# Optimization experiments

Measured on AMD Instinct MI355X. Metric: run time of the kernel, lower is better.

Reference implementation:

```python
import jax, jax.numpy as jnp
import numpy as np

B, T, D = 64, 512, 1024
VOCAB = 50257


def setup_inputs() -> dict:
    key = jax.random.key(0)
    k1, k2, k3, k4 = jax.random.split(key, 4)
    vector_sequence = jax.random.normal(k1, (B, T, D), dtype=jnp.float32)
    # lengths in [1, T] to avoid degenerate all-zero rows (divide-by-zero, as in torch)
    sentence_length = jax.random.randint(k2, (B,), 1, T + 1, dtype=jnp.int32)
    word_sequence = jax.random.randint(k3, (B, T), 0, VOCAB, dtype=jnp.int32)
    # original init: 0.1 - 0.2*U[0,1) -> uniform in (-0.1, 0.1]
    weights = 0.1 - 0.2 * jax.random.uniform(k4, (VOCAB,), dtype=jnp.float32)
    return {
        "vector_sequence": vector_sequence,
        "sentence_length": sentence_length,
        "word_sequence": word_sequence,
        "weights": weights,
    }


def reference(vector_sequence, sentence_length, word_sequence, weights):
    # mask positions >= sentence_length (in-place zeroing in the original)
    mask = (jnp.arange(T)[None, :] < sentence_length[:, None]).astype(vector_sequence.dtype)  # [B,T]
    vs = vector_sequence * mask[:, :, None]  # [B,T,D]
    s = jnp.sum(vs, axis=1)  # [B,D]
    y = s / jnp.sqrt(jnp.sum(jnp.abs(s), axis=1, keepdims=True))  # [B,D]
    # per-token scalar weight gather, scale, masked sum over T
    w = weights[word_sequence] * mask  # [B,T]
    y_hat = jnp.einsum('btd,bt->bd', vs, w)  # [B,D]
    return (y, y_hat)
```

## Files before the change

kernel.cpp:

```cpp
#include <hip/hip_runtime.h>
#include <math.h>

constexpr int B = 64;
constexpr int T = 512;
constexpr int D = 1024;
constexpr int NT = 16;
constexpr int CHUNK = T / NT;


__global__ __launch_bounds__(256) void k1_partial(
    const float* __restrict__ vs,
    const int*   __restrict__ slen,
    const int*   __restrict__ words,
    const float* __restrict__ wts,
    float*       __restrict__ part)
{
    const int bid = blockIdx.x;
    const int b  = bid & (B - 1);
    const int tc = bid >> 6;
    const int len = slen[b];
    const int t0 = tc * CHUNK;
    if (t0 >= len) return;
    const int t1 = (t0 + CHUNK < len) ? (t0 + CHUNK) : len;

    __shared__ float wbuf[CHUNK];
    const int tid = threadIdx.x;
    if (tid < CHUNK) {
        const int t = t0 + tid;
        wbuf[tid] = (t < len) ? wts[words[b * T + t]] : 0.0f;
    }
    __syncthreads();

    const int d0 = tid * 4;
    const float4* vp = (const float4*)(vs + ((size_t)(b * T + t0)) * D + d0);
    float4 s  = make_float4(0.f, 0.f, 0.f, 0.f);
    float4 yh = make_float4(0.f, 0.f, 0.f, 0.f);

    #pragma unroll 4
    for (int t = t0; t < t1; ++t) {
        const float4 v = *vp;
        vp += D / 4;
        const float w = wbuf[t - t0];
        s.x += v.x; s.y += v.y; s.z += v.z; s.w += v.w;
        yh.x += v.x * w; yh.y += v.y * w; yh.z += v.z * w; yh.w += v.w * w;
    }

    float* p = part + ((size_t)tc * B + b) * (2 * D) + d0;
    *(float4*)p       = s;
    *(float4*)(p + D) = yh;
}

__global__ __launch_bounds__(256) void k2_finalize(
    const float* __restrict__ part,
    const int*   __restrict__ slen,
    float*       __restrict__ out)
{
    const int b = blockIdx.x;
    const int tid = threadIdx.x;
    const int len = slen[b];
    const int nact = (len + CHUNK - 1) / CHUNK;

    const int d0 = tid * 4;
    float4 s  = make_float4(0.f, 0.f, 0.f, 0.f);
    float4 yh = make_float4(0.f, 0.f, 0.f, 0.f);
    for (int tc = 0; tc < nact; ++tc) {
        const float* p = part + ((size_t)tc * B + b) * (2 * D) + d0;
        const float4 ps = *(const float4*)p;
        const float4 py = *(const float4*)(p + D);
        s.x += ps.x; s.y += ps.y; s.z += ps.z; s.w += ps.w;
        yh.x += py.x; yh.y += py.y; yh.z += py.z; yh.w += py.w;
    }

    float a = fabsf(s.x) + fabsf(s.y) + fabsf(s.z) + fabsf(s.w);
    for (int off = 32; off > 0; off >>= 1)
        a += __shfl_down(a, off, 64);

    __shared__ float psum[4];
    const int wave = tid >> 6;
    const int lane = tid & 63;
    if (lane == 0) psum[wave] = a;
    __syncthreads();
    const float tot = psum[0] + psum[1] + psum[2] + psum[3];
    const float inv = 1.0f / sqrtf(tot);

    float4 y;
    y.x = s.x * inv; y.y = s.y * inv; y.z = s.z * inv; y.w = s.w * inv;
    *(float4*)(out + (size_t)b * D + d0)       = y;
    *(float4*)(out + (size_t)(B + b) * D + d0) = yh;
}

extern "C" void kernel_launch(void* const* d_in, const int* in_sizes, int n_in,
                              void* d_out, int out_size, void* d_ws, size_t ws_size,
                              hipStream_t stream) {
    const float* vs    = (const float*)d_in[0];
    const int*   slen  = (const int*)  d_in[1];
    const int*   words = (const int*)  d_in[2];
    const float* wts   = (const float*)d_in[3];
    float* out  = (float*)d_out;
    float* part = (float*)d_ws;

    k1_partial <<<B * NT, 256, 0, stream>>>(vs, slen, words, wts, part);
    k2_finalize<<<B,      256, 0, stream>>>(part, slen, out);
}
```

Baseline: 185.1 us.

## Fuse finalize into partial kernel via last-block atomic ticket and nontemporal loads

Replaces the separate finalize kernel with a last-block-done pattern. Each block writes its partial sums, fences, and takes an atomic ticket per batch row, and the last-arriving block for that row reduces all partials and writes the outputs. A tiny init kernel zeroes the counters. Vector loads of the input become nontemporal to avoid cache pollution. The goal is to remove the serialized tail kernel's launch gap, at the cost of fences, atomics and an extra small launch.

```diff
diff --git a/kernel.cpp b/kernel.cpp
--- a/kernel.cpp
+++ b/kernel.cpp
@@ -6,24 +6,36 @@
 constexpr int D = 1024;
 constexpr int NT = 16;
 constexpr int CHUNK = T / NT;
+constexpr size_t PART_ELEMS = (size_t)NT * B * 2 * D;
+
+typedef float f32x4 __attribute__((ext_vector_type(4)));
 
 
-__global__ __launch_bounds__(256) void k1_partial(
+__global__ __launch_bounds__(64) void k0_init(int* __restrict__ cnt) {
+    cnt[threadIdx.x] = 0;
+}
+
+__global__ __launch_bounds__(256) void k_fused(
     const float* __restrict__ vs,
     const int*   __restrict__ slen,
     const int*   __restrict__ words,
     const float* __restrict__ wts,
-    float*       __restrict__ part)
+    float*       __restrict__ part,
+    int*         __restrict__ cnt,
+    float*       __restrict__ out)
 {
     const int bid = blockIdx.x;
-    const int b  = bid & (B - 1);
-    const int tc = bid >> 6;
+    const int b   = bid & (B - 1);
+    const int tc  = bid >> 6;
     const int len = slen[b];
+    const int nact = (len + CHUNK - 1) / CHUNK;
+    if (tc >= nact) return;
+
     const int t0 = tc * CHUNK;
-    if (t0 >= len) return;
     const int t1 = (t0 + CHUNK < len) ? (t0 + CHUNK) : len;
 
     __shared__ float wbuf[CHUNK];
+    __shared__ int   ticket;
     const int tid = threadIdx.x;
     if (tid < CHUNK) {
         const int t = t0 + tid;
@@ -32,46 +44,42 @@
     __syncthreads();
 
     const int d0 = tid * 4;
-    const float4* vp = (const float4*)(vs + ((size_t)(b * T + t0)) * D + d0);
-    float4 s  = make_float4(0.f, 0.f, 0.f, 0.f);
-    float4 yh = make_float4(0.f, 0.f, 0.f, 0.f);
+    const f32x4* vp = (const f32x4*)(vs + ((size_t)(b * T + t0)) * D + d0);
+    f32x4 s  = {0.f, 0.f, 0.f, 0.f};
+    f32x4 yh = {0.f, 0.f, 0.f, 0.f};
 
     #pragma unroll 4
     for (int t = t0; t < t1; ++t) {
-        const float4 v = *vp;
+        const f32x4 v = __builtin_nontemporal_load(vp);
         vp += D / 4;
         const float w = wbuf[t - t0];
-        s.x += v.x; s.y += v.y; s.z += v.z; s.w += v.w;
-        yh.x += v.x * w; yh.y += v.y * w; yh.z += v.z * w; yh.w += v.w * w;
+        s  += v;
+        yh += v * w;
     }
 
     float* p = part + ((size_t)tc * B + b) * (2 * D) + d0;
-    *(float4*)p       = s;
-    *(float4*)(p + D) = yh;
-}
+    *(f32x4*)p       = s;
+    *(f32x4*)(p + D) = yh;
 
-__global__ __launch_bounds__(256) void k2_finalize(
-    const float* __restrict__ part,
-    const int*   __restrict__ slen,
-    float*       __restrict__ out)
-{
-    const int b = blockIdx.x;
-    const int tid = threadIdx.x;
-    const int len = slen[b];
-    const int nact = (len + CHUNK - 1) / CHUNK;
+    __threadfence();
+    __syncthreads();
+    if (tid == 0) ticket = atomicAdd(&cnt[b], 1);
+    __syncthreads();
+    if (ticket != nact - 1) return;
 
-    const int d0 = tid * 4;
-    float4 s  = make_float4(0.f, 0.f, 0.f, 0.f);
-    float4 yh = make_float4(0.f, 0.f, 0.f, 0.f);
-    for (int tc = 0; tc < nact; ++tc) {
-        const float* p = part + ((size_t)tc * B + b) * (2 * D) + d0;
-        const float4 ps = *(const float4*)p;
-        const float4 py = *(const float4*)(p + D);
-        s.x += ps.x; s.y += ps.y; s.z += ps.z; s.w += ps.w;
-        yh.x += py.x; yh.y += py.y; yh.z += py.z; yh.w += py.w;
+    __threadfence();
+
+    f32x4 S  = {0.f, 0.f, 0.f, 0.f};
+    f32x4 YH = {0.f, 0.f, 0.f, 0.f};
+    for (int c = 0; c < nact; ++c) {
+        const float* q = part + ((size_t)c * B + b) * (2 * D) + d0;
+        const f32x4 ps = *(const f32x4*)q;
+        const f32x4 py = *(const f32x4*)(q + D);
+        S  += ps;
+        YH += py;
     }
 
-    float a = fabsf(s.x) + fabsf(s.y) + fabsf(s.z) + fabsf(s.w);
+    float a = fabsf(S.x) + fabsf(S.y) + fabsf(S.z) + fabsf(S.w);
     for (int off = 32; off > 0; off >>= 1)
         a += __shfl_down(a, off, 64);
 
@@ -83,10 +91,9 @@
     const float tot = psum[0] + psum[1] + psum[2] + psum[3];
     const float inv = 1.0f / sqrtf(tot);
 
-    float4 y;
-    y.x = s.x * inv; y.y = s.y * inv; y.z = s.z * inv; y.w = s.w * inv;
-    *(float4*)(out + (size_t)b * D + d0)       = y;
-    *(float4*)(out + (size_t)(B + b) * D + d0) = yh;
+    f32x4 y = S * inv;
+    *(f32x4*)(out + (size_t)b * D + d0)       = y;
+    *(f32x4*)(out + (size_t)(B + b) * D + d0) = YH;
 }
 
 extern "C" void kernel_launch(void* const* d_in, const int* in_sizes, int n_in,
@@ -98,7 +105,8 @@
     const float* wts   = (const float*)d_in[3];
     float* out  = (float*)d_out;
     float* part = (float*)d_ws;
+    int*   cnt  = (int*)(part + PART_ELEMS);
 
-    k1_partial <<<B * NT, 256, 0, stream>>>(vs, slen, words, wts, part);
-    k2_finalize<<<B,      256, 0, stream>>>(part, slen, out);
+    k0_init<<<1,      64,  0, stream>>>(cnt);
+    k_fused<<<B * NT, 256, 0, stream>>>(vs, slen, words, wts, part, cnt, out);
 }
```

Result: slower. 297.7 us (+60.9%).
